# Kernel optimization log

Measured on AMD Instinct MI355X. Metric: run time of the kernel, lower is better.

The kernel has to match this reference:

```python
import jax, jax.numpy as jnp
import numpy as np

B, T, C, H = 2, 2048, 1024, 16  # batch, seq (== block_size), n_embd, n_head
HD = C // H  # head dim


def setup_inputs() -> dict:
    key = jax.random.key(0)
    k1, k2, k3 = jax.random.split(key, 3)
    x = jax.random.normal(k1, (B, T, C), dtype=jnp.float32)
    w_attn = jax.random.normal(k2, (C, 3 * C), dtype=jnp.float32) * (1.0 / np.sqrt(C))
    b_attn = jnp.zeros((3 * C,), dtype=jnp.float32)
    w_proj = jax.random.normal(k3, (C, C), dtype=jnp.float32) * (1.0 / np.sqrt(C))
    b_proj = jnp.zeros((C,), dtype=jnp.float32)
    return {"x": x, "w_attn": w_attn, "b_attn": b_attn, "w_proj": w_proj, "b_proj": b_proj}


def reference(x, w_attn, b_attn, w_proj, b_proj):
    # qkv projection: [B,T,3C]
    qkv = x @ w_attn + b_attn
    q, k, v = jnp.split(qkv, 3, axis=-1)
    # -> [B,H,T,HD]
    def to_heads(t):
        return t.reshape(B, T, H, HD).transpose(0, 2, 1, 3)
    q, k, v = to_heads(q), to_heads(k), to_heads(v)
    scale = 1.0 / np.sqrt(HD).astype(np.float32)
    # att: [B,H,T,T]
    att = jnp.einsum("bhqd,bhkd->bhqk", q, k) * scale
    causal = jnp.tril(jnp.ones((T, T), dtype=bool))
    att = jnp.where(causal[None, None], att, -jnp.inf)
    att = jax.nn.softmax(att, axis=-1)
    # y: [B,H,T,HD] -> [B,T,C]
    y = jnp.einsum("bhqk,bhkd->bhqd", att, v)
    y = y.transpose(0, 2, 1, 3).reshape(B, T, C)
    return y @ w_proj + b_proj
```

## Files before the change

kernel.cpp:

```cpp
#include <hip/hip_runtime.h>
#include <stdint.h>

#define Bb 2
#define Tt 2048
#define Cc 1024
#define Hh 16
#define HD 64
#define C3 3072

typedef __bf16 bf16x8 __attribute__((ext_vector_type(8)));
typedef float  f32x4  __attribute__((ext_vector_type(4)));
typedef unsigned short u16;
typedef u16 u16x8 __attribute__((ext_vector_type(8)));
typedef u16 u16x4 __attribute__((ext_vector_type(4)));

#define SCALE2 0.18033688f

__device__ __forceinline__ u16 f2bf(float f) {
  union { float f; unsigned u; } v; v.f = f;
  return (u16)((v.u + 0x7fffu + ((v.u >> 16) & 1u)) >> 16);
}
__device__ __forceinline__ u16 f2bf_fast(float f) {
  union { float f; unsigned u; } v; v.f = f;
  return (u16)((v.u + 0x8000u) >> 16);
}
__device__ __forceinline__ float bf2f(u16 a) {
  union { unsigned u; float f; } v; v.u = ((unsigned)a) << 16; return v.f;
}

__device__ __forceinline__ void gl2lds16(const void* g, void* s) {
  __builtin_amdgcn_global_load_lds(
      (__attribute__((address_space(1))) void*)(g),
      (__attribute__((address_space(3))) void*)(s), 16, 0, 0);
}

__device__ __forceinline__ bf16x8 ldb8(const u16* p) {
  return __builtin_bit_cast(bf16x8, *(const u16x8*)p);
}

__global__ void cvt_x_kernel(const float* __restrict__ in, u16* __restrict__ out, int n4) {
  int i = blockIdx.x * blockDim.x + threadIdx.x;
  if (i < n4) {
    float4 v = ((const float4*)in)[i];
    u16x4 o = { f2bf(v.x), f2bf(v.y), f2bf(v.z), f2bf(v.w) };
    ((u16x4*)out)[i] = o;
  }
}

__global__ void transpose_cvt(const float* __restrict__ in, u16* __restrict__ out,
                              int R, int C) {
  __shared__ u16 tile[64][65];
  int c0 = blockIdx.x * 64, r0 = blockIdx.y * 64;
  int x = threadIdx.x & 63, y = threadIdx.x >> 6;
  #pragma unroll
  for (int rr = y; rr < 64; rr += 4)
    tile[rr][x] = f2bf(in[(size_t)(r0 + rr) * C + c0 + x]);
  __syncthreads();
  #pragma unroll
  for (int rr = y; rr < 64; rr += 4)
    out[(size_t)(c0 + rr) * R + r0 + x] = tile[x][rr];
}

template <int MODE, int BN>
__global__ __launch_bounds__(256)
void gemm_bt(const u16* __restrict__ A, const u16* __restrict__ Bt,
             const float* __restrict__ bias, void* __restrict__ Cout,
             u16* __restrict__ Vt, int M, int N, int K) {
  __shared__ u16 As[128 * 64];
  __shared__ u16 Bs[BN * 64];
  constexpr int JT = BN / 32;
  const int tid = threadIdx.x;
  const int ln  = tid & 63;
  const int w   = tid >> 6;
  const int wm  = w >> 1, wn = w & 1;
  const int l15 = ln & 15, lq = ln >> 4;
  const int swz = l15 & 7;
  const int m0 = blockIdx.y * 128, n0 = blockIdx.x * BN;

  f32x4 acc[4][JT];
  #pragma unroll
  for (int i = 0; i < 4; ++i)
    #pragma unroll
    for (int j = 0; j < JT; ++j)
      acc[i][j] = (f32x4){0.f, 0.f, 0.f, 0.f};

  for (int k0 = 0; k0 < K; k0 += 64) {
    #pragma unroll
    for (int i = 0; i < 4; ++i) {
      int s = i * 256 + tid;
      int row = s >> 3, cg = s & 7;
      gl2lds16(A + (size_t)(m0 + row) * K + k0 + ((cg ^ (row & 7)) * 8),
               (char*)As + (size_t)(i * 256 + w * 64) * 16);
    }
    #pragma unroll
    for (int i = 0; i < BN / 32; ++i) {
      int s = i * 256 + tid;
      int row = s >> 3, cg = s & 7;
      gl2lds16(Bt + (size_t)(n0 + row) * K + k0 + ((cg ^ (row & 7)) * 8),
               (char*)Bs + (size_t)(i * 256 + w * 64) * 16);
    }
    __syncthreads();
    #pragma unroll
    for (int ho = 0; ho < 2; ++ho) {
      bf16x8 af[4], bfr[JT];
      #pragma unroll
      for (int i = 0; i < 4; ++i)
        af[i] = ldb8(&As[(wm * 64 + i * 16 + l15) * 64 + ((ho * 4 + lq) ^ swz) * 8]);
      #pragma unroll
      for (int j = 0; j < JT; ++j)
        bfr[j] = ldb8(&Bs[(wn * (BN / 2) + j * 16 + l15) * 64 + ((ho * 4 + lq) ^ swz) * 8]);
      #pragma unroll
      for (int i = 0; i < 4; ++i)
        #pragma unroll
        for (int j = 0; j < JT; ++j)
          acc[i][j] = __builtin_amdgcn_mfma_f32_16x16x32_bf16(af[i], bfr[j], acc[i][j], 0, 0, 0);
    }
    __syncthreads();
  }

  if (MODE == 1 && n0 >= 2048) {
    #pragma unroll
    for (int i = 0; i < 4; ++i) {
      int rowb = m0 + wm * 64 + i * 16 + lq * 4;
      int b_ = rowb >> 11, t0 = rowb & 2047;
      #pragma unroll
      for (int j = 0; j < JT; ++j) {
        int col = n0 + wn * (BN / 2) + j * 16 + l15;
        int hd = col - 2048;
        float bsv = bias[col];
        u16x4 pk;
        #pragma unroll
        for (int r = 0; r < 4; ++r) pk[r] = f2bf(acc[i][j][r] + bsv);
        *(u16x4*)&Vt[(size_t)(b_ * 1024 + hd) * Tt + t0] = pk;
      }
    }
  } else {
    const int ldc = (MODE == 1) ? 2048 : N;
    #pragma unroll
    for (int i = 0; i < 4; ++i) {
      int row = m0 + wm * 64 + i * 16 + lq * 4;
      #pragma unroll
      for (int j = 0; j < JT; ++j) {
        int col = n0 + wn * (BN / 2) + j * 16 + l15;
        float bsv = bias[col];
        #pragma unroll
        for (int r = 0; r < 4; ++r) {
          float v = acc[i][j][r] + bsv;
          if (MODE == 1) ((u16*)Cout)[(size_t)(row + r) * ldc + col] = f2bf(v);
          else           ((float*)Cout)[(size_t)(row + r) * ldc + col] = v;
        }
      }
    }
  }
}


__device__ __forceinline__ bf16x8 packp(const f32x4& a, const f32x4& b) {
  u16x8 u = { f2bf_fast(a[0]), f2bf_fast(a[1]), f2bf_fast(a[2]), f2bf_fast(a[3]),
              f2bf_fast(b[0]), f2bf_fast(b[1]), f2bf_fast(b[2]), f2bf_fast(b[3]) };
  return __builtin_bit_cast(bf16x8, u);
}
__device__ __forceinline__ bf16x8 qscale(const u16* p) {
  u16x8 q = *(const u16x8*)p;
  u16x8 s;
  #pragma unroll
  for (int j = 0; j < 8; ++j) s[j] = f2bf(bf2f(q[j]) * SCALE2);
  return __builtin_bit_cast(bf16x8, s);
}

__global__ __launch_bounds__(256, 4)
void attn_fused(const u16* __restrict__ qk, const u16* __restrict__ vt,
                u16* __restrict__ y) {
  __shared__ u16 Ks[64 * 64];
  __shared__ u16 Vts[64 * 64];
  const int tid = threadIdx.x;
  const int ln = tid & 63, w = tid >> 6;
  const int l15 = ln & 15, lq = ln >> 4;
  const int swz = l15 & 7;
  const int bx = blockIdx.x;
  const int bh = bx & 31;
  const int h  = bh & 15, b = bh >> 4;
  const int rr_ = bx >> 8, g = (bx >> 5) & 7;
  const int qt = (rr_ == 0) ? 31 - g : (rr_ == 1) ? 16 + g : (rr_ == 2) ? 15 - g : g;
  const int q0 = qt * 64;
  const int q0w = q0 + w * 16;

  const u16* qbase = qk + (size_t)(b * Tt) * 2048 + h * HD;
  const u16* kbase = qk + (size_t)(b * Tt) * 2048 + 1024 + h * HD;
  const u16* vbase = vt + (size_t)(b * 1024 + h * HD) * Tt;

  const int s0 = tid, s1 = 256 + tid;
  const int koff0 = (s0 >> 3) * 2048 + (((s0 & 7) ^ ((s0 >> 3) & 7)) * 8);
  const int koff1 = (s1 >> 3) * 2048 + (((s1 & 7) ^ ((s1 >> 3) & 7)) * 8);
  char* kd0 = (char*)Ks  + w * 1024;
  char* kd1 = (char*)Ks  + 4096 + w * 1024;
  char* vd0 = (char*)Vts + w * 1024;
  char* vd1 = (char*)Vts + 4096 + w * 1024;

  const u16* qrA = qbase + (size_t)(q0w + l15) * 2048;
  bf16x8 qA0 = qscale(qrA + lq * 8), qA1 = qscale(qrA + 32 + lq * 8);

  f32x4 o[4];
  #pragma unroll
  for (int j = 0; j < 4; ++j) o[j] = (f32x4){0,0,0,0};
  float m = -__builtin_inff(), l = 0.f;
  const int qg = q0w + l15;

  const int nkv = qt + 1;
  for (int it = 0; it < nkv; ++it) {
    const int kk = it * 64;
    __syncthreads();
    {
      const u16* ksrc = kbase + (size_t)kk * 2048;
      const u16* vsrc = vbase + kk;
      gl2lds16(ksrc + koff0, kd0);
      gl2lds16(ksrc + koff1, kd1);
      gl2lds16(vsrc + koff0, vd0);
      gl2lds16(vsrc + koff1, vd1);
    }
    __syncthreads();

    f32x4 t[4];
    #pragma unroll
    for (int i = 0; i < 4; ++i) t[i] = (f32x4){0,0,0,0};
    #pragma unroll
    for (int i = 0; i < 4; ++i) {
      bf16x8 kf0 = ldb8(&Ks[(i * 16 + l15) * 64 + ((lq    ) ^ swz) * 8]);
      bf16x8 kf1 = ldb8(&Ks[(i * 16 + l15) * 64 + ((lq + 4) ^ swz) * 8]);
      t[i] = __builtin_amdgcn_mfma_f32_16x16x32_bf16(kf0, qA0, t[i], 0, 0, 0);
      t[i] = __builtin_amdgcn_mfma_f32_16x16x32_bf16(kf1, qA1, t[i], 0, 0, 0);
    }

    const bool lastI = (it == nkv - 1);
    if (lastI) {
      #pragma unroll
      for (int i = 0; i < 4; ++i)
        #pragma unroll
        for (int r = 0; r < 4; ++r) {
          int kv = kk + i * 16 + lq * 4 + r;
          if (kv > qg) t[i][r] = -__builtin_inff();
        }
    }
    float mx = t[0][0];
    #pragma unroll
    for (int i = 0; i < 4; ++i)
      #pragma unroll
      for (int r = 0; r < 4; ++r) mx = fmaxf(mx, t[i][r]);
    mx = fmaxf(mx, __shfl_xor(mx, 16));
    mx = fmaxf(mx, __shfl_xor(mx, 32));
    float mn = fmaxf(m, mx);
    float al = __builtin_amdgcn_exp2f(m - mn);
    float ps = 0.f;
    #pragma unroll
    for (int i = 0; i < 4; ++i)
      #pragma unroll
      for (int r = 0; r < 4; ++r) {
        float p = __builtin_amdgcn_exp2f(t[i][r] - mn);
        t[i][r] = p;
        ps += p;
      }
    ps += __shfl_xor(ps, 16);
    ps += __shfl_xor(ps, 32);
    l = l * al + ps;
    m = mn;
    #pragma unroll
    for (int jd = 0; jd < 4; ++jd)
      #pragma unroll
      for (int r = 0; r < 4; ++r) o[jd][r] *= al;

    bf16x8 p0 = packp(t[0], t[1]), p1 = packp(t[2], t[3]);
    #pragma unroll
    for (int mf = 0; mf < 2; ++mf) {
      bf16x8 pb = mf ? p1 : p0;
      #pragma unroll
      for (int jd = 0; jd < 4; ++jd) {
        int d = jd * 16 + l15;
        int plo = ((mf * 4     + (lq >> 1)) ^ swz);
        int phi = ((mf * 4 + 2 + (lq >> 1)) ^ swz);
        u16x4 a = *(const u16x4*)&Vts[d * 64 + plo * 8 + (lq & 1) * 4];
        u16x4 c = *(const u16x4*)&Vts[d * 64 + phi * 8 + (lq & 1) * 4];
        u16x8 u = { a[0], a[1], a[2], a[3], c[0], c[1], c[2], c[3] };
        o[jd] = __builtin_amdgcn_mfma_f32_16x16x32_bf16(
                    __builtin_bit_cast(bf16x8, u), pb, o[jd], 0, 0, 0);
      }
    }
  }

  float inv = 1.f / l;
  const size_t ybase = (size_t)(b * Tt + q0w + l15) * Cc + h * HD;
  #pragma unroll
  for (int jd = 0; jd < 4; ++jd) {
    u16x4 pk;
    #pragma unroll
    for (int r = 0; r < 4; ++r) pk[r] = f2bf(o[jd][r] * inv);
    *(u16x4*)&y[ybase + jd * 16 + lq * 4] = pk;
  }
}

extern "C" void kernel_launch(void* const* d_in, const int* in_sizes, int n_in,
                              void* d_out, int out_size, void* d_ws, size_t ws_size,
                              hipStream_t stream) {
  const float* x      = (const float*)d_in[0];
  const float* w_attn = (const float*)d_in[1];
  const float* b_attn = (const float*)d_in[2];
  const float* w_proj = (const float*)d_in[3];
  const float* b_proj = (const float*)d_in[4];
  float* out = (float*)d_out;

  char* ws = (char*)d_ws;
  u16* xb  = (u16*)(ws + 0);
  u16* wat = (u16*)(ws + 8388608);
  u16* wpt = (u16*)(ws + 14680064);
  u16* qkb = (u16*)(ws + 16777216);
  u16* vtb = (u16*)(ws + 33554432);
  u16* yb  = (u16*)(ws + 41943040);

  cvt_x_kernel<<<4096, 256, 0, stream>>>(x, xb, 1048576);
  transpose_cvt<<<dim3(48, 16), 256, 0, stream>>>(w_attn, wat, 1024, 3072);
  transpose_cvt<<<dim3(16, 16), 256, 0, stream>>>(w_proj, wpt, 1024, 1024);
  gemm_bt<1, 128><<<dim3(24, 32), 256, 0, stream>>>(xb, wat, b_attn, (void*)qkb, vtb, 4096, 3072, 1024);
  attn_fused<<<1024, 256, 0, stream>>>(qkb, vtb, yb);
  gemm_bt<0, 64><<<dim3(16, 32), 256, 0, stream>>>(yb, wpt, b_proj, (void*)out, nullptr, 4096, 1024, 1024);
}
```

Measured before the change: 196.9 us.

## Double-buffer attention K/V tiles, permute V^T layout, fuse prep kernels

Attention now keeps two LDS buffers for the K and V^T tiles and prefetches the next tile with global_load_lds while computing the current one, dropping one barrier per iteration. The QKV GEMM writes V^T in a permuted order within each 64-column block, so the PV MFMA operand becomes a single 16-byte LDS read instead of two 8-byte reads plus a repack. The x conversion and the two weight transposes are merged into one launch to cut launch overhead. Correctness depends on the compiler waiting on the async loads before the barrier, and on the permuted V^T layout matching the read pattern.

```diff
diff --git a/kernel.cpp b/kernel.cpp
--- a/kernel.cpp
+++ b/kernel.cpp
@@ -38,27 +38,38 @@
   return __builtin_bit_cast(bf16x8, *(const u16x8*)p);
 }
 
-__global__ void cvt_x_kernel(const float* __restrict__ in, u16* __restrict__ out, int n4) {
-  int i = blockIdx.x * blockDim.x + threadIdx.x;
-  if (i < n4) {
-    float4 v = ((const float4*)in)[i];
+__global__ __launch_bounds__(256)
+void prep_kernel(const float* __restrict__ x, const float* __restrict__ w_attn,
+                 const float* __restrict__ w_proj, u16* __restrict__ xb,
+                 u16* __restrict__ wat, u16* __restrict__ wpt) {
+  __shared__ u16 tile[64][65];
+  const int blk = blockIdx.x;
+  const int tid = threadIdx.x;
+  if (blk < 4096) {
+    int i = blk * 256 + tid;
+    float4 v = ((const float4*)x)[i];
     u16x4 o = { f2bf(v.x), f2bf(v.y), f2bf(v.z), f2bf(v.w) };
-    ((u16x4*)out)[i] = o;
-  }
-}
-
-__global__ void transpose_cvt(const float* __restrict__ in, u16* __restrict__ out,
-                              int R, int C) {
-  __shared__ u16 tile[64][65];
-  int c0 = blockIdx.x * 64, r0 = blockIdx.y * 64;
-  int x = threadIdx.x & 63, y = threadIdx.x >> 6;
-  #pragma unroll
-  for (int rr = y; rr < 64; rr += 4)
-    tile[rr][x] = f2bf(in[(size_t)(r0 + rr) * C + c0 + x]);
+    ((u16x4*)xb)[i] = o;
+    return;
+  }
+  const float* in; u16* out; int R, C, c0, r0;
+  if (blk < 4096 + 768) {
+    int t = blk - 4096;
+    in = w_attn; out = wat; R = 1024; C = 3072;
+    c0 = (t % 48) * 64; r0 = (t / 48) * 64;
+  } else {
+    int t = blk - 4864;
+    in = w_proj; out = wpt; R = 1024; C = 1024;
+    c0 = (t & 15) * 64; r0 = (t >> 4) * 64;
+  }
+  int xx = tid & 63, yy = tid >> 6;
+  #pragma unroll
+  for (int rr = yy; rr < 64; rr += 4)
+    tile[rr][xx] = f2bf(in[(size_t)(r0 + rr) * C + c0 + xx]);
   __syncthreads();
   #pragma unroll
-  for (int rr = y; rr < 64; rr += 4)
-    out[(size_t)(c0 + rr) * R + r0 + x] = tile[x][rr];
+  for (int rr = yy; rr < 64; rr += 4)
+    out[(size_t)(c0 + rr) * R + r0 + xx] = tile[xx][rr];
 }
 
 template <int MODE, int BN>
@@ -123,6 +134,10 @@
     for (int i = 0; i < 4; ++i) {
       int rowb = m0 + wm * 64 + i * 16 + lq * 4;
       int b_ = rowb >> 11, t0 = rowb & 2047;
+      int tl = t0 & 63;
+      int c = tl >> 4, ll = (tl >> 2) & 3;
+      int pos0 = (c >> 1) * 32 + ll * 8 + (c & 1) * 4;
+      size_t tdst = (size_t)(t0 & ~63) + pos0;
       #pragma unroll
       for (int j = 0; j < JT; ++j) {
         int col = n0 + wn * (BN / 2) + j * 16 + l15;
@@ -131,7 +146,7 @@
         u16x4 pk;
         #pragma unroll
         for (int r = 0; r < 4; ++r) pk[r] = f2bf(acc[i][j][r] + bsv);
-        *(u16x4*)&Vt[(size_t)(b_ * 1024 + hd) * Tt + t0] = pk;
+        *(u16x4*)&Vt[(size_t)(b_ * 1024 + hd) * Tt + tdst] = pk;
       }
     }
   } else {
@@ -171,8 +186,8 @@
 __global__ __launch_bounds__(256, 4)
 void attn_fused(const u16* __restrict__ qk, const u16* __restrict__ vt,
                 u16* __restrict__ y) {
-  __shared__ u16 Ks[64 * 64];
-  __shared__ u16 Vts[64 * 64];
+  __shared__ u16 Ks[2][64 * 64];
+  __shared__ u16 Vts[2][64 * 64];
   const int tid = threadIdx.x;
   const int ln = tid & 63, w = tid >> 6;
   const int l15 = ln & 15, lq = ln >> 4;
@@ -192,10 +207,6 @@
   const int s0 = tid, s1 = 256 + tid;
   const int koff0 = (s0 >> 3) * 2048 + (((s0 & 7) ^ ((s0 >> 3) & 7)) * 8);
   const int koff1 = (s1 >> 3) * 2048 + (((s1 & 7) ^ ((s1 >> 3) & 7)) * 8);
-  char* kd0 = (char*)Ks  + w * 1024;
-  char* kd1 = (char*)Ks  + 4096 + w * 1024;
-  char* vd0 = (char*)Vts + w * 1024;
-  char* vd1 = (char*)Vts + 4096 + w * 1024;
 
   const u16* qrA = qbase + (size_t)(q0w + l15) * 2048;
   bf16x8 qA0 = qscale(qrA + lq * 8), qA1 = qscale(qrA + 32 + lq * 8);
@@ -207,26 +218,38 @@
   const int qg = q0w + l15;
 
   const int nkv = qt + 1;
+
+  {
+    const u16* ksrc = kbase;
+    const u16* vsrc = vbase;
+    gl2lds16(ksrc + koff0, (char*)Ks[0] + w * 1024);
+    gl2lds16(ksrc + koff1, (char*)Ks[0] + 4096 + w * 1024);
+    gl2lds16(vsrc + koff0, (char*)Vts[0] + w * 1024);
+    gl2lds16(vsrc + koff1, (char*)Vts[0] + 4096 + w * 1024);
+  }
+
   for (int it = 0; it < nkv; ++it) {
     const int kk = it * 64;
+    const int p = it & 1;
     __syncthreads();
-    {
-      const u16* ksrc = kbase + (size_t)kk * 2048;
-      const u16* vsrc = vbase + kk;
-      gl2lds16(ksrc + koff0, kd0);
-      gl2lds16(ksrc + koff1, kd1);
-      gl2lds16(vsrc + koff0, vd0);
-      gl2lds16(vsrc + koff1, vd1);
-    }
-    __syncthreads();
+    if (it + 1 < nkv) {
+      const u16* ksrc = kbase + (size_t)(kk + 64) * 2048;
+      const u16* vsrc = vbase + kk + 64;
+      gl2lds16(ksrc + koff0, (char*)Ks[p ^ 1] + w * 1024);
+      gl2lds16(ksrc + koff1, (char*)Ks[p ^ 1] + 4096 + w * 1024);
+      gl2lds16(vsrc + koff0, (char*)Vts[p ^ 1] + w * 1024);
+      gl2lds16(vsrc + koff1, (char*)Vts[p ^ 1] + 4096 + w * 1024);
+    }
+    const u16* KsB  = Ks[p];
+    const u16* VtsB = Vts[p];
 
     f32x4 t[4];
     #pragma unroll
     for (int i = 0; i < 4; ++i) t[i] = (f32x4){0,0,0,0};
     #pragma unroll
     for (int i = 0; i < 4; ++i) {
-      bf16x8 kf0 = ldb8(&Ks[(i * 16 + l15) * 64 + ((lq    ) ^ swz) * 8]);
-      bf16x8 kf1 = ldb8(&Ks[(i * 16 + l15) * 64 + ((lq + 4) ^ swz) * 8]);
+      bf16x8 kf0 = ldb8(&KsB[(i * 16 + l15) * 64 + ((lq    ) ^ swz) * 8]);
+      bf16x8 kf1 = ldb8(&KsB[(i * 16 + l15) * 64 + ((lq + 4) ^ swz) * 8]);
       t[i] = __builtin_amdgcn_mfma_f32_16x16x32_bf16(kf0, qA0, t[i], 0, 0, 0);
       t[i] = __builtin_amdgcn_mfma_f32_16x16x32_bf16(kf1, qA1, t[i], 0, 0, 0);
     }
@@ -255,9 +278,9 @@
     for (int i = 0; i < 4; ++i)
       #pragma unroll
       for (int r = 0; r < 4; ++r) {
-        float p = __builtin_amdgcn_exp2f(t[i][r] - mn);
-        t[i][r] = p;
-        ps += p;
+        float pp = __builtin_amdgcn_exp2f(t[i][r] - mn);
+        t[i][r] = pp;
+        ps += pp;
       }
     ps += __shfl_xor(ps, 16);
     ps += __shfl_xor(ps, 32);
@@ -275,13 +298,8 @@
       #pragma unroll
       for (int jd = 0; jd < 4; ++jd) {
         int d = jd * 16 + l15;
-        int plo = ((mf * 4     + (lq >> 1)) ^ swz);
-        int phi = ((mf * 4 + 2 + (lq >> 1)) ^ swz);
-        u16x4 a = *(const u16x4*)&Vts[d * 64 + plo * 8 + (lq & 1) * 4];
-        u16x4 c = *(const u16x4*)&Vts[d * 64 + phi * 8 + (lq & 1) * 4];
-        u16x8 u = { a[0], a[1], a[2], a[3], c[0], c[1], c[2], c[3] };
-        o[jd] = __builtin_amdgcn_mfma_f32_16x16x32_bf16(
-                    __builtin_bit_cast(bf16x8, u), pb, o[jd], 0, 0, 0);
+        bf16x8 vf = ldb8(&VtsB[d * 64 + ((mf * 4 + lq) ^ swz) * 8]);
+        o[jd] = __builtin_amdgcn_mfma_f32_16x16x32_bf16(vf, pb, o[jd], 0, 0, 0);
       }
     }
   }
@@ -315,9 +333,7 @@
   u16* vtb = (u16*)(ws + 33554432);
   u16* yb  = (u16*)(ws + 41943040);
 
-  cvt_x_kernel<<<4096, 256, 0, stream>>>(x, xb, 1048576);
-  transpose_cvt<<<dim3(48, 16), 256, 0, stream>>>(w_attn, wat, 1024, 3072);
-  transpose_cvt<<<dim3(16, 16), 256, 0, stream>>>(w_proj, wpt, 1024, 1024);
+  prep_kernel<<<5120, 256, 0, stream>>>(x, w_attn, w_proj, xb, wat, wpt);
   gemm_bt<1, 128><<<dim3(24, 32), 256, 0, stream>>>(xb, wat, b_attn, (void*)qkb, vtb, 4096, 3072, 1024);
   attn_fused<<<1024, 256, 0, stream>>>(qkb, vtb, yb);
   gemm_bt<0, 64><<<dim3(16, 32), 256, 0, stream>>>(yb, wpt, b_proj, (void*)out, nullptr, 4096, 1024, 1024);
```

Result: faster. 186.2 us (-5.4%).
